# Kernel tuning notes

Hardware: AMD Instinct MI355X
Metric: run time of the kernel (lower is better)

Reference implementation:

```python
import jax, jax.numpy as jnp
from jax import lax
import numpy as np

PARAM_SPECS = [
    ("w1", (16, 15, 5, 5)), ("b1", (16,)),
    ("w2", (32, 16, 3, 3)), ("b2", (32,)),
    ("w3", (32, 32, 3, 3)), ("b3", (32,)),
    ("w4", (32, 32, 3, 3)), ("b4", (32,)),
    ("w5", (64, 32, 3, 3)), ("b5", (64,)),
    ("w6", (32, 96, 3, 3)), ("b6", (32,)),
    ("w7", (32, 64, 3, 3)), ("b7", (32,)),
    ("w8", (32, 64, 3, 3)), ("b8", (32,)),
    ("w9", (64, 48, 3, 3)), ("b9", (64,)),
    ("wi", (16, 15, 3, 3)), ("bi", (16,)),
    ("wo", (3, 16, 3, 3)), ("bo", (3,)),
]


def conv2d(x, w, b, pad):
    y = lax.conv_general_dilated(x, w, (1, 1), [(pad, pad), (pad, pad)],
                                 dimension_numbers=("NCHW", "OIHW", "NCHW"))
    return y + b[None, :, None, None]


def maxpool2(x):
    return lax.reduce_window(x, -jnp.inf, lax.max, (1, 1, 2, 2), (1, 1, 2, 2), "VALID")


def upsample(x, hw):
    # bilinear, half-pixel centers == torch align_corners=False
    B, C = x.shape[:2]
    return jax.image.resize(x, (B, C, hw[0], hw[1]), method="bilinear")


def dcnn(img, p):
    x1 = jax.nn.relu(conv2d(img, p["w1"], p["b1"], 2))
    x2 = jax.nn.relu(conv2d(maxpool2(x1), p["w2"], p["b2"], 1))
    x3 = jax.nn.relu(conv2d(maxpool2(x2), p["w3"], p["b3"], 1))
    x4 = jax.nn.relu(conv2d(maxpool2(x3), p["w4"], p["b4"], 1))
    x5 = jax.nn.relu(conv2d(maxpool2(x4), p["w5"], p["b5"], 1))
    x6 = jax.nn.relu(conv2d(jnp.concatenate([upsample(x5, x4.shape[-2:]), x4], 1), p["w6"], p["b6"], 1))
    x7 = jax.nn.relu(conv2d(jnp.concatenate([upsample(x6, x3.shape[-2:]), x3], 1), p["w7"], p["b7"], 1))
    x8 = jax.nn.relu(conv2d(jnp.concatenate([upsample(x7, x2.shape[-2:]), x2], 1), p["w8"], p["b8"], 1))
    x9 = conv2d(jnp.concatenate([upsample(x8, x1.shape[-2:]), x1], 1), p["w9"], p["b9"], 1)
    return x9


def lrnn_op(X, P, axis, flip):
    # h_k = (1-P_k)*X_k + P_k*h_{k-1}, scanned along `axis`.
    # For reverse directions the torch code stacks hidden states in scan
    # order (spatially flipped) -> flip inputs, scan forward, keep order.
    if flip:
        X = jnp.flip(X, axis)
        P = jnp.flip(P, axis)
    xs = jnp.moveaxis(X, axis, 0)  # [L, B, 16, n]
    ps = jnp.moveaxis(P, axis, 0)

    def step(h, xp):
        x, p = xp
        h = (1.0 - p) * x + p * h
        return h, h

    h0 = jnp.zeros_like(xs[0])
    _, ys = lax.scan(step, h0, (xs, ps))
    return jnp.moveaxis(ys, 0, axis)


def lrnn_layer(x_in, fm):
    dirs = [(0, 3, False), (0, 3, True), (16, 2, False), (16, 2, True),
            (32, 3, False), (32, 3, True), (48, 2, False), (48, 2, True)]
    outs = [lrnn_op(x_in, fm[:, c:c + 16], axis, flip) for (c, axis, flip) in dirs]
    return jnp.max(jnp.stack(outs, axis=1), axis=1)


def setup_inputs() -> dict:
    key = jax.random.key(0)
    ks = jax.random.split(key, len(PARAM_SPECS) + 1)
    inp = {"img": jax.random.normal(ks[0], (8, 15, 256, 256), jnp.float32)}
    for i, (name, shape) in enumerate(PARAM_SPECS):
        inp[name] = jax.random.normal(ks[i + 1], shape, jnp.float32) * 0.05
    return inp


def reference(img, w1, b1, w2, b2, w3, b3, w4, b4, w5, b5, w6, b6, w7, b7,
              w8, b8, w9, b9, wi, bi, wo, bo):
    p = dict(w1=w1, b1=b1, w2=w2, b2=b2, w3=w3, b3=b3, w4=w4, b4=b4, w5=w5,
             b5=b5, w6=w6, b6=b6, w7=w7, b7=b7, w8=w8, b8=b8, w9=w9, b9=b9)
    fm = jnp.tanh(dcnn(img, p))          # [B,64,H,W]
    x_in = conv2d(img, wi, bi, 1)         # [B,16,H,W]
    out = lrnn_layer(x_in, fm)            # [B,16,H,W]
    return jax.nn.sigmoid(conv2d(out, wo, bo, 1))  # [B,3,H,W]
```

## Files before the change

kernel.cpp:

```cpp
#include <hip/hip_runtime.h>
#include <math.h>

typedef __attribute__((ext_vector_type(8)))  short bf16x8;
typedef __attribute__((ext_vector_type(8)))  unsigned short u16x8;
typedef __attribute__((ext_vector_type(16))) float f32x16;

__device__ __forceinline__ unsigned short f2bf(float f) {
    unsigned u = __float_as_uint(f);
    unsigned r = (u + 0x7FFFu + ((u >> 16) & 1u)) >> 16;
    return (unsigned short)r;
}
__device__ __forceinline__ float bf2f(unsigned short h) {
    return __uint_as_float(((unsigned)h) << 16);
}
__device__ __forceinline__ unsigned pack2(unsigned short a, unsigned short b) {
    return (unsigned)a | ((unsigned)b << 16);
}
__device__ __forceinline__ float fast_tanh(float x) {
    float e = __expf(2.f * x);
    return 1.f - 2.f / (e + 1.f);
}

__device__ __forceinline__ void bilin_setup(int y, int x, int Hi, int Wi,
                                            int& i00, int& i01, int& i10, int& i11,
                                            float& wy, float& wx)
{
    float fy = 0.5f * y - 0.25f;
    float fx = 0.5f * x - 0.25f;
    float y0f = floorf(fy), x0f = floorf(fx);
    wy = fy - y0f; wx = fx - x0f;
    int yA = (int)y0f, xA = (int)x0f;
    int yB = yA + 1, xB = xA + 1;
    yA = yA < 0 ? 0 : (yA > Hi - 1 ? Hi - 1 : yA);
    yB = yB < 0 ? 0 : (yB > Hi - 1 ? Hi - 1 : yB);
    xA = xA < 0 ? 0 : (xA > Wi - 1 ? Wi - 1 : xA);
    xB = xB < 0 ? 0 : (xB > Wi - 1 ? Wi - 1 : xB);
    i00 = yA * Wi + xA; i01 = yA * Wi + xB;
    i10 = yB * Wi + xA; i11 = yB * Wi + xB;
}

__device__ __forceinline__ void up2_setup(int v, int Hi, int& i0, int& i1, float& w)
{
    int a = (v - 1) >> 1;
    i0 = a < 0 ? 0 : a;
    int b = a + 1;
    i1 = b > Hi - 1 ? Hi - 1 : b;
    w = (v & 1) ? 0.25f : 0.75f;
}

__device__ __forceinline__ u16x8 bilin8(const unsigned short* __restrict__ sb,
                                        int i00, int i01, int i10, int i11,
                                        float wy, float wx, int stride)
{
    u16x8 v00 = *(const u16x8*)(sb + (size_t)i00 * stride);
    u16x8 v01 = *(const u16x8*)(sb + (size_t)i01 * stride);
    u16x8 v10 = *(const u16x8*)(sb + (size_t)i10 * stride);
    u16x8 v11 = *(const u16x8*)(sb + (size_t)i11 * stride);
    float w00 = (1.f - wy) * (1.f - wx), w01 = (1.f - wy) * wx;
    float w10 = wy * (1.f - wx),         w11 = wy * wx;
    u16x8 r;
#pragma unroll
    for (int j = 0; j < 8; ++j)
        r[j] = f2bf(w00 * bf2f(v00[j]) + w01 * bf2f(v01[j]) +
                    w10 * bf2f(v10[j]) + w11 * bf2f(v11[j]));
    return r;
}

__global__ void imgT_bf16(const float* __restrict__ img, unsigned short* __restrict__ dst)
{
    int idx = blockIdx.x * 256 + threadIdx.x;
    if (idx >= 8 * 256 * 256) return;
    int x = idx & 255, y = (idx >> 8) & 255, b = idx >> 16;
    unsigned short v[16];
#pragma unroll
    for (int c = 0; c < 15; ++c)
        v[c] = f2bf(img[(size_t)(b * 15 + c) * 65536 + y * 256 + x]);
    v[15] = 0;
    uint4 lo = make_uint4(pack2(v[0], v[1]), pack2(v[2], v[3]), pack2(v[4], v[5]), pack2(v[6], v[7]));
    uint4 hi = make_uint4(pack2(v[8], v[9]), pack2(v[10], v[11]), pack2(v[12], v[13]), pack2(v[14], v[15]));
    *(uint4*)(dst + (size_t)idx * 16)     = lo;
    *(uint4*)(dst + (size_t)idx * 16 + 8) = hi;
}

__device__ __forceinline__ void pack33(const float* __restrict__ w,
                                       unsigned short* __restrict__ dst,
                                       int i, int Cin, int Cout)
{
    int KST = Cin >> 4, MT = Cout >> 5;
    int j = i & 7;
    int lane = (i >> 3) & 63;
    int t = i >> 9;
    int mt = t % MT; t /= MT;
    int kst = t % KST;
    int s = t / KST;
    int oc = mt * 32 + (lane & 31);
    int ci = kst * 16 + (lane >> 5) * 8 + j;
    dst[i] = f2bf(w[(oc * Cin + ci) * 9 + s]);
}

__global__ void wprep_mega(const float* __restrict__ w9, const float* __restrict__ w8,
                           const float* __restrict__ w1, const float* __restrict__ wi,
                           const float* __restrict__ wo, const float* __restrict__ w2,
                           const float* __restrict__ w3, const float* __restrict__ w4,
                           const float* __restrict__ w5, const float* __restrict__ w6,
                           const float* __restrict__ w7,
                           unsigned short* __restrict__ wpk9, unsigned short* __restrict__ wpk8,
                           unsigned short* __restrict__ wpk1, unsigned short* __restrict__ wpki,
                           unsigned short* __restrict__ wpko, unsigned short* __restrict__ wpk2,
                           unsigned short* __restrict__ wpk3, unsigned short* __restrict__ wpk4,
                           unsigned short* __restrict__ wpk5, unsigned short* __restrict__ wpk6,
                           unsigned short* __restrict__ wpk7)
{
    int idx = blockIdx.x * 256 + threadIdx.x;
    if (idx < 27648)       pack33(w9, wpk9, idx, 48, 64);
    else if (idx < 46080)  pack33(w8, wpk8, idx - 27648, 64, 32);
    else if (idx < 58880) {
        int i = idx - 46080;
        int j = i & 7;
        int lane = (i >> 3) & 63;
        int s = i >> 9;
        int oc = lane & 31;
        int ci = (lane >> 5) * 8 + j;
        float v = 0.f;
        if (oc < 16 && ci < 15) v = w1[((oc * 15 + ci) * 5 + s / 5) * 5 + s % 5];
        wpk1[i] = f2bf(v);
    } else if (idx < 63488) {
        int i = idx - 58880;
        int j = i & 7;
        int lane = (i >> 3) & 63;
        int s = i >> 9;
        int oc = lane & 31;
        int ci = (lane >> 5) * 8 + j;
        float v = 0.f;
        if (oc < 16 && ci < 15) v = wi[((oc * 15 + ci) * 3 + s / 3) * 3 + s % 3];
        wpki[i] = f2bf(v);
    } else if (idx < 68096) {
        int i = idx - 63488;
        int j = i & 7;
        int lane = (i >> 3) & 63;
        int s = i >> 9;
        int oc = lane & 31;
        int ci = (lane >> 5) * 8 + j;
        float v = 0.f;
        if (oc < 3) v = wo[((oc * 16 + ci) * 3 + s / 3) * 3 + s % 3];
        wpko[i] = f2bf(v);
    }
    else if (idx < 72704)  pack33(w2, wpk2, idx - 68096, 16, 32);
    else if (idx < 81920)  pack33(w3, wpk3, idx - 72704, 32, 32);
    else if (idx < 91136)  pack33(w4, wpk4, idx - 81920, 32, 32);
    else if (idx < 109568) pack33(w5, wpk5, idx - 91136, 32, 64);
    else if (idx < 137216) pack33(w6, wpk6, idx - 109568, 96, 32);
    else if (idx < 155648) pack33(w7, wpk7, idx - 137216, 64, 32);
}

template<int CIN, int COUT, int H, int W, int ROWS, int POOL>
__global__ __launch_bounds__(256)
void convN_mfma(const unsigned short* __restrict__ in,
                const unsigned short* __restrict__ wpk,
                const float* __restrict__ bias,
                unsigned short* __restrict__ out)
{
    constexpr int G = CIN / 8;
    constexpr int KST = CIN / 16;
    constexpr int MT = COUT / 32;
    constexpr int TR = ROWS + 2;
    constexpr int TWd = W + 2;
    constexpr int PS = TR * TWd * 8 + 8;
    __shared__ __align__(16) unsigned short smem[G * PS];

    const int tid  = threadIdx.x;
    const int lane = tid & 63;
    const int wv   = tid >> 6;
    const int q    = lane >> 5;
    const int y0   = blockIdx.x * ROWS;
    const int b    = blockIdx.y;

    for (int i = tid; i < G * TR * TWd; i += 256) {
        int g = i % G;
        int u = (i / G) % TWd;
        int t = i / (G * TWd);
        int yg = y0 + t - 1, xg = u - 1;
        u16x8 v = {0, 0, 0, 0, 0, 0, 0, 0};
        if (yg >= 0 && yg < H && xg >= 0 && xg < W) {
            if (POOL) {
                const unsigned short* q0 =
                    in + (((size_t)(b * 2 * H + 2 * yg) * 2 * W + 2 * xg) * CIN + g * 8);
                u16x8 a0 = *(const u16x8*)q0;
                u16x8 a1 = *(const u16x8*)(q0 + CIN);
                u16x8 a2 = *(const u16x8*)(q0 + (size_t)2 * W * CIN);
                u16x8 a3 = *(const u16x8*)(q0 + (size_t)2 * W * CIN + CIN);
#pragma unroll
                for (int j = 0; j < 8; ++j)
                    v[j] = f2bf(fmaxf(fmaxf(bf2f(a0[j]), bf2f(a1[j])),
                                      fmaxf(bf2f(a2[j]), bf2f(a3[j]))));
            } else {
                v = *(const u16x8*)(in + (((size_t)(b * H + yg) * W + xg) * CIN + g * 8));
            }
        }
        *(u16x8*)(&smem[g * PS + (t * TWd + u) * 8]) = v;
    }
    __syncthreads();

    const int p = wv * 32 + (lane & 31);
    const int r = p / W;
    const int x = p % W;

    f32x16 acc[MT];
#pragma unroll
    for (int mt = 0; mt < MT; ++mt)
#pragma unroll
        for (int i = 0; i < 16; ++i) acc[mt][i] = 0.f;

    const unsigned short* wbase = wpk + lane * 8;

#pragma unroll
    for (int s = 0; s < 9; ++s) {
        const int dy = s / 3, dx = s % 3;
#pragma unroll
        for (int kst = 0; kst < KST; ++kst) {
            const int g = kst * 2 + q;
            bf16x8 bfrag = *(const bf16x8*)(&smem[g * PS + ((r + dy) * TWd + (x + dx)) * 8]);
#pragma unroll
            for (int mt = 0; mt < MT; ++mt) {
                bf16x8 a = *(const bf16x8*)(wbase + ((s * KST + kst) * MT + mt) * 512);
                acc[mt] = __builtin_amdgcn_mfma_f32_32x32x16_bf16(a, bfrag, acc[mt], 0, 0, 0);
            }
        }
    }

    size_t base = ((size_t)(b * H + y0 + r) * W + x) * COUT;
#pragma unroll
    for (int mt = 0; mt < MT; ++mt)
#pragma unroll
        for (int rg = 0; rg < 4; ++rg) {
            int oc = mt * 32 + 8 * rg + 4 * q;
            unsigned short s0 = f2bf(fmaxf(acc[mt][rg * 4 + 0] + bias[oc + 0], 0.f));
            unsigned short s1 = f2bf(fmaxf(acc[mt][rg * 4 + 1] + bias[oc + 1], 0.f));
            unsigned short s2 = f2bf(fmaxf(acc[mt][rg * 4 + 2] + bias[oc + 2], 0.f));
            unsigned short s3 = f2bf(fmaxf(acc[mt][rg * 4 + 3] + bias[oc + 3], 0.f));
            *(uint2*)(out + base + oc) = make_uint2(pack2(s0, s1), pack2(s2, s3));
        }
}

template<int UPC, int CSKIP, int COUT, int H, int W, int ROWS>
__global__ __launch_bounds__(256)
void convU_mfma(const unsigned short* __restrict__ up,
                const unsigned short* __restrict__ skip,
                const unsigned short* __restrict__ wpk,
                const float* __restrict__ bias,
                unsigned short* __restrict__ out)
{
    constexpr int CIN = UPC + CSKIP;
    constexpr int G = CIN / 8;
    constexpr int GU = UPC / 8;
    constexpr int KST = CIN / 16;
    constexpr int MT = COUT / 32;
    constexpr int TR = ROWS + 2;
    constexpr int TWd = W + 2;
    constexpr int PS = TR * TWd * 8 + 8;
    __shared__ __align__(16) unsigned short smem[G * PS];

    const int tid  = threadIdx.x;
    const int lane = tid & 63;
    const int wv   = tid >> 6;
    const int q    = lane >> 5;
    const int y0   = blockIdx.x * ROWS;
    const int b    = blockIdx.y;

    for (int i = tid; i < G * TR * TWd; i += 256) {
        int g = i % G;
        int u = (i / G) % TWd;
        int t = i / (G * TWd);
        int yg = y0 + t - 1, xg = u - 1;
        u16x8 v = {0, 0, 0, 0, 0, 0, 0, 0};
        if (yg >= 0 && yg < H && xg >= 0 && xg < W) {
            if (g < GU) {
                int i00, i01, i10, i11; float wy, wx;
                bilin_setup(yg, xg, H / 2, W / 2, i00, i01, i10, i11, wy, wx);
                v = bilin8(up + (size_t)b * (H / 2) * (W / 2) * UPC + g * 8,
                           i00, i01, i10, i11, wy, wx, UPC);
            } else {
                v = *(const u16x8*)(skip + (((size_t)(b * H + yg) * W + xg) * CSKIP
                                            + (g - GU) * 8));
            }
        }
        *(u16x8*)(&smem[g * PS + (t * TWd + u) * 8]) = v;
    }
    __syncthreads();

    const int p = wv * 32 + (lane & 31);
    const int r = p / W;
    const int x = p % W;

    f32x16 acc[MT];
#pragma unroll
    for (int mt = 0; mt < MT; ++mt)
#pragma unroll
        for (int i = 0; i < 16; ++i) acc[mt][i] = 0.f;

    const unsigned short* wbase = wpk + lane * 8;

#pragma unroll
    for (int s = 0; s < 9; ++s) {
        const int dy = s / 3, dx = s % 3;
#pragma unroll
        for (int kst = 0; kst < KST; ++kst) {
            const int g = kst * 2 + q;
            bf16x8 bfrag = *(const bf16x8*)(&smem[g * PS + ((r + dy) * TWd + (x + dx)) * 8]);
#pragma unroll
            for (int mt = 0; mt < MT; ++mt) {
                bf16x8 a = *(const bf16x8*)(wbase + ((s * KST + kst) * MT + mt) * 512);
                acc[mt] = __builtin_amdgcn_mfma_f32_32x32x16_bf16(a, bfrag, acc[mt], 0, 0, 0);
            }
        }
    }

    size_t base = ((size_t)(b * H + y0 + r) * W + x) * COUT;
#pragma unroll
    for (int mt = 0; mt < MT; ++mt)
#pragma unroll
        for (int rg = 0; rg < 4; ++rg) {
            int oc = mt * 32 + 8 * rg + 4 * q;
            unsigned short s0 = f2bf(fmaxf(acc[mt][rg * 4 + 0] + bias[oc + 0], 0.f));
            unsigned short s1 = f2bf(fmaxf(acc[mt][rg * 4 + 1] + bias[oc + 1], 0.f));
            unsigned short s2 = f2bf(fmaxf(acc[mt][rg * 4 + 2] + bias[oc + 2], 0.f));
            unsigned short s3 = f2bf(fmaxf(acc[mt][rg * 4 + 3] + bias[oc + 3], 0.f));
            *(uint2*)(out + base + oc) = make_uint2(pack2(s0, s1), pack2(s2, s3));
        }
}

__global__ __launch_bounds__(256)
void conv1i_mfma(const unsigned short* __restrict__ imgT,
                 const unsigned short* __restrict__ wpk1,
                 const unsigned short* __restrict__ wpki,
                 const float* __restrict__ b1, const float* __restrict__ bi,
                 unsigned short* __restrict__ x1t, unsigned short* __restrict__ xin)
{
    __shared__ __align__(16) unsigned short smem[2 * 5 * 132 * 8];

    const int tid  = threadIdx.x;
    const int lane = tid & 63;
    const int wv   = tid >> 6;
    const int n    = lane & 31;
    const int q    = lane >> 5;
    const int y    = blockIdx.x >> 1;
    const int x0   = (blockIdx.x & 1) * 128;
    const int b    = blockIdx.y;

    for (int i = tid; i < 5 * 132 * 2; i += 256) {
        int r   = i / 264;
        int rem = i - r * 264;
        int xi  = rem >> 1;
        int g   = rem & 1;
        int yg = y + r - 2;
        int xg = x0 - 2 + xi;
        uint4 v = make_uint4(0, 0, 0, 0);
        if (yg >= 0 && yg < 256 && xg >= 0 && xg < 256)
            v = *(const uint4*)(imgT + (((size_t)(b * 256 + yg) * 256 + xg) * 16 + g * 8));
        *(uint4*)(&smem[((g * 5 + r) * 132 + xi) * 8]) = v;
    }
    __syncthreads();

    f32x16 acc1, acci;
#pragma unroll
    for (int i = 0; i < 16; ++i) { acc1[i] = 0.f; acci[i] = 0.f; }

    const int pxl = wv * 32 + n;
    const unsigned short* wb1 = wpk1 + lane * 8;
    const unsigned short* wbi = wpki + lane * 8;

#pragma unroll
    for (int s = 0; s < 25; ++s) {
        const int dy = s / 5, dx = s % 5;
        bf16x8 bfrag = *(const bf16x8*)(&smem[((q * 5 + dy) * 132 + pxl + dx) * 8]);
        bf16x8 a = *(const bf16x8*)(wb1 + s * 512);
        acc1 = __builtin_amdgcn_mfma_f32_32x32x16_bf16(a, bfrag, acc1, 0, 0, 0);
    }
#pragma unroll
    for (int s = 0; s < 9; ++s) {
        const int dy = s / 3, dx = s % 3;
        bf16x8 bfrag = *(const bf16x8*)(&smem[((q * 5 + dy + 1) * 132 + pxl + dx + 1) * 8]);
        bf16x8 a = *(const bf16x8*)(wbi + s * 512);
        acci = __builtin_amdgcn_mfma_f32_32x32x16_bf16(a, bfrag, acci, 0, 0, 0);
    }

    const int px = x0 + pxl;
    size_t base1 = ((size_t)(b * 256 + y) * 256 + px) * 16;
#pragma unroll
    for (int rg = 0; rg < 2; ++rg) {
        int oc = 8 * rg + 4 * q;
        unsigned short s0 = f2bf(fmaxf(acc1[rg * 4 + 0] + b1[oc + 0], 0.f));
        unsigned short s1 = f2bf(fmaxf(acc1[rg * 4 + 1] + b1[oc + 1], 0.f));
        unsigned short s2 = f2bf(fmaxf(acc1[rg * 4 + 2] + b1[oc + 2], 0.f));
        unsigned short s3 = f2bf(fmaxf(acc1[rg * 4 + 3] + b1[oc + 3], 0.f));
        *(uint2*)(x1t + base1 + oc) = make_uint2(pack2(s0, s1), pack2(s2, s3));
    }
#pragma unroll
    for (int reg = 0; reg < 8; ++reg) {
        int row = (reg & 3) + 8 * (reg >> 2) + 4 * q;
        xin[((size_t)(b * 16 + row) * 256 + y) * 256 + px] = f2bf(acci[reg] + bi[row]);
    }
}

__global__ __launch_bounds__(256)
void conv8_mfma(const unsigned short* __restrict__ x7t,
                const unsigned short* __restrict__ x2t,
                const unsigned short* __restrict__ wpk8,
                const float* __restrict__ bias,
                unsigned short* __restrict__ x8t)
{
    constexpr int PS8 = 4 * 66 * 8 + 8;
    __shared__ __align__(16) unsigned short smem[8 * PS8];

    const int tid  = threadIdx.x;
    const int lane = tid & 63;
    const int wv   = tid >> 6;
    const int n    = lane & 31;
    const int q    = lane >> 5;
    const int x0   = (blockIdx.x & 1) * 64;
    const int yp   = blockIdx.x >> 1;
    const int b    = blockIdx.y;

    for (int i = tid; i < 8 * 4 * 66; i += 256) {
        int t   = i / 528;
        int rem = i - t * 528;
        int xi  = rem >> 3;
        int g   = rem & 7;
        int yg = 2 * yp + t - 1;
        int xg = x0 - 1 + xi;
        u16x8 v = {0, 0, 0, 0, 0, 0, 0, 0};
        if (yg >= 0 && yg < 128 && xg >= 0 && xg < 128) {
            if (g < 4) {
                int iy0, iy1, ix0, ix1; float wy, wx;
                up2_setup(yg, 64, iy0, iy1, wy);
                up2_setup(xg, 64, ix0, ix1, wx);
                v = bilin8(x7t + (size_t)b * 64 * 64 * 32 + g * 8,
                           iy0 * 64 + ix0, iy0 * 64 + ix1,
                           iy1 * 64 + ix0, iy1 * 64 + ix1, wy, wx, 32);
            } else {
                v = *(const u16x8*)(x2t + (((size_t)(b * 128 + yg) * 128 + xg) * 32
                                           + (g - 4) * 8));
            }
        }
        *(u16x8*)(&smem[g * PS8 + (t * 66 + xi) * 8]) = v;
    }
    __syncthreads();

    const int rr  = wv >> 1;
    const int pxl = (wv & 1) * 32 + n;

    f32x16 acc;
#pragma unroll
    for (int i = 0; i < 16; ++i) acc[i] = 0.f;

    const unsigned short* wbase = wpk8 + lane * 8;

#pragma unroll
    for (int s = 0; s < 9; ++s) {
        const int dy = s / 3, dx = s % 3;
#pragma unroll
        for (int kst = 0; kst < 4; ++kst) {
            const int g = kst * 2 + q;
            bf16x8 bfrag = *(const bf16x8*)(&smem[g * PS8 + ((rr + dy) * 66 + pxl + dx) * 8]);
            bf16x8 a = *(const bf16x8*)(wbase + (s * 4 + kst) * 512);
            acc = __builtin_amdgcn_mfma_f32_32x32x16_bf16(a, bfrag, acc, 0, 0, 0);
        }
    }

    size_t base = ((size_t)(b * 128 + 2 * yp + rr) * 128 + x0 + pxl) * 32;
#pragma unroll
    for (int rg = 0; rg < 4; ++rg) {
        int oc0 = 8 * rg + 4 * q;
        unsigned short s0 = f2bf(fmaxf(acc[rg * 4 + 0] + bias[oc0 + 0], 0.f));
        unsigned short s1 = f2bf(fmaxf(acc[rg * 4 + 1] + bias[oc0 + 1], 0.f));
        unsigned short s2 = f2bf(fmaxf(acc[rg * 4 + 2] + bias[oc0 + 2], 0.f));
        unsigned short s3 = f2bf(fmaxf(acc[rg * 4 + 3] + bias[oc0 + 3], 0.f));
        *(uint2*)(x8t + base + oc0) = make_uint2(pack2(s0, s1), pack2(s2, s3));
    }
}

__global__ __launch_bounds__(256)
void conv9f_mfma(const unsigned short* __restrict__ x8t,
                 const unsigned short* __restrict__ x1t,
                 const unsigned short* __restrict__ wpk,
                 const float* __restrict__ bias,
                 unsigned short* __restrict__ fm)
{
    constexpr int PS9 = 4 * 66 * 8 + 8;
    __shared__ __align__(16) unsigned short smem[6 * PS9];

    const int tid  = threadIdx.x;
    const int lane = tid & 63;
    const int wv   = tid >> 6;
    const int n    = lane & 31;
    const int q    = lane >> 5;
    const int x0   = (blockIdx.x & 3) * 64;
    const int yp   = blockIdx.x >> 2;
    const int b    = blockIdx.y;

    for (int i = tid; i < 6 * 4 * 66; i += 256) {
        int t   = i / 396;
        int rem = i - t * 396;
        int xi  = rem / 6;
        int g   = rem - xi * 6;
        int yg = 2 * yp + t - 1;
        int xg = x0 - 1 + xi;
        u16x8 v = {0, 0, 0, 0, 0, 0, 0, 0};
        if (yg >= 0 && yg < 256 && xg >= 0 && xg < 256) {
            if (g < 4) {
                int iy0, iy1, ix0, ix1; float wy, wx;
                up2_setup(yg, 128, iy0, iy1, wy);
                up2_setup(xg, 128, ix0, ix1, wx);
                v = bilin8(x8t + (size_t)b * 128 * 128 * 32 + g * 8,
                           iy0 * 128 + ix0, iy0 * 128 + ix1,
                           iy1 * 128 + ix0, iy1 * 128 + ix1, wy, wx, 32);
            } else {
                v = *(const u16x8*)(x1t + (((size_t)(b * 256 + yg) * 256 + xg) * 16 + (g - 4) * 8));
            }
        }
        *(u16x8*)(&smem[g * PS9 + (t * 66 + xi) * 8]) = v;
    }
    __syncthreads();

    const int rr  = wv >> 1;
    const int pxl = (wv & 1) * 32 + n;

    f32x16 acc0, acc1;
#pragma unroll
    for (int i = 0; i < 16; ++i) { acc0[i] = 0.f; acc1[i] = 0.f; }

    const unsigned short* wbase = wpk + lane * 8;

#pragma unroll
    for (int s = 0; s < 9; ++s) {
        const int dy = s / 3, dx = s % 3;
#pragma unroll
        for (int kst = 0; kst < 3; ++kst) {
            const int g = kst * 2 + q;
            bf16x8 bfrag = *(const bf16x8*)(&smem[g * PS9 + ((rr + dy) * 66 + pxl + dx) * 8]);
            bf16x8 a0 = *(const bf16x8*)(wbase + ((s * 3 + kst) * 2 + 0) * 512);
            bf16x8 a1 = *(const bf16x8*)(wbase + ((s * 3 + kst) * 2 + 1) * 512);
            acc0 = __builtin_amdgcn_mfma_f32_32x32x16_bf16(a0, bfrag, acc0, 0, 0, 0);
            acc1 = __builtin_amdgcn_mfma_f32_32x32x16_bf16(a1, bfrag, acc1, 0, 0, 0);
        }
    }

    __syncthreads();
    unsigned short* lout = smem;
    const int pb = rr * 64 + pxl + q * 512;
#pragma unroll
    for (int reg = 0; reg < 16; ++reg) {
        const int rbase = (reg & 3) + 8 * (reg >> 2);
        lout[rbase * 128 + pb]        = f2bf(fast_tanh(acc0[reg] + bias[rbase + 4 * q]));
        lout[(rbase + 32) * 128 + pb] = f2bf(fast_tanh(acc1[reg] + bias[rbase + 4 * q + 32]));
    }
    __syncthreads();

    const size_t fmb = (size_t)b * 64 * 65536 + (size_t)(2 * yp) * 256 + x0;
    for (int i = tid; i < 1024; i += 256) {
        int oc  = i >> 4;
        int p0  = (i & 15) * 8;
        int rr2 = p0 >> 6;
        int pl  = p0 & 63;
        uint4 v = *(const uint4*)(lout + oc * 128 + p0);
        *(uint4*)(fm + fmb + (size_t)oc * 65536 + rr2 * 256 + pl) = v;
    }
}

__device__ __forceinline__ int X2C(int x) { return x + (x >> 5); }

__global__ __launch_bounds__(256)
void lrnn_w_seg(const unsigned short* __restrict__ X, const unsigned short* __restrict__ FM,
                unsigned short* __restrict__ rnnW)
{
    __shared__ float tx[3][16][264];
    __shared__ unsigned short outm[2][16][256];
    __shared__ float segres[2][16][8][4];
    __shared__ float hin[2][16][8][2];

    const int tid = threadIdx.x;
    const int bid = blockIdx.x;
    const int yt = bid & 15;
    const int c  = (bid >> 4) & 15;
    const int b  = bid >> 8;
    const int y0 = yt * 16;

    const size_t xb  = ((size_t)(b * 16 + c) * 256 + y0) * 256;
    const size_t p1b = ((size_t)(b * 64 + c) * 256 + y0) * 256;
    const size_t p2b = ((size_t)(b * 64 + 32 + c) * 256 + y0) * 256;

    for (int i = tid; i < 1536; i += 256) {
        int s = i >> 9;
        int r = i & 511;
        int y = r >> 5;
        int g = r & 31;
        const unsigned short* sp = (s == 0) ? (X + xb) : (s == 1 ? FM + p1b : FM + p2b);
        u16x8 v = *(const u16x8*)(sp + (size_t)y * 256 + g * 8);
        int c0 = X2C(g * 8);
#pragma unroll
        for (int j = 0; j < 8; ++j) tx[s][y][c0 + j] = bf2f(v[j]);
    }
    __syncthreads();

    const int y  = tid & 15;
    const int sg = (tid >> 4) & 7;
    const int d  = tid >> 7;

    {
        float h1 = 0.f, h2 = 0.f, A1 = 1.f, A2 = 1.f;
        if (d == 0) {
            int cs = X2C(sg * 32);
#pragma unroll
            for (int i = 0; i < 32; ++i) {
                float xv = tx[0][y][cs + i], p1 = tx[1][y][cs + i], p2 = tx[2][y][cs + i];
                h1 = fmaf(p1, h1 - xv, xv); A1 *= p1;
                h2 = fmaf(p2, h2 - xv, xv); A2 *= p2;
            }
        } else {
            int cs = X2C(255 - sg * 32);
#pragma unroll
            for (int i = 0; i < 32; ++i) {
                float xv = tx[0][y][cs - i], p1 = tx[1][y][cs - i], p2 = tx[2][y][cs - i];
                h1 = fmaf(p1, h1 - xv, xv); A1 *= p1;
                h2 = fmaf(p2, h2 - xv, xv); A2 *= p2;
            }
        }
        segres[d][y][sg][0] = h1; segres[d][y][sg][1] = A1;
        segres[d][y][sg][2] = h2; segres[d][y][sg][3] = A2;
    }
    __syncthreads();

    if (tid < 32) {
        int yy = tid & 15, dd = tid >> 4;
        float c1 = 0.f, c2 = 0.f;
        for (int s = 0; s < 8; ++s) {
            hin[dd][yy][s][0] = c1;
            hin[dd][yy][s][1] = c2;
            c1 = segres[dd][yy][s][0] + segres[dd][yy][s][1] * c1;
            c2 = segres[dd][yy][s][2] + segres[dd][yy][s][3] * c2;
        }
    }
    __syncthreads();

    {
        float h1 = hin[d][y][sg][0], h2 = hin[d][y][sg][1];
        if (d == 0) {
            int cs = X2C(sg * 32);
            int xs = sg * 32;
#pragma unroll
            for (int i = 0; i < 32; ++i) {
                float xv = tx[0][y][cs + i], p1 = tx[1][y][cs + i], p2 = tx[2][y][cs + i];
                h1 = fmaf(p1, h1 - xv, xv);
                h2 = fmaf(p2, h2 - xv, xv);
                outm[0][y][xs + i] = f2bf(fmaxf(h1, h2));
            }
        } else {
            int cs = X2C(255 - sg * 32);
#pragma unroll
            for (int i = 0; i < 32; ++i) {
                int t = sg * 32 + i;
                float xv = tx[0][y][cs - i], p1 = tx[1][y][cs - i], p2 = tx[2][y][cs - i];
                h1 = fmaf(p1, h1 - xv, xv);
                h2 = fmaf(p2, h2 - xv, xv);
                outm[1][y][t] = f2bf(fmaxf(h1, h2));
            }
        }
    }
    __syncthreads();

    for (int i = tid; i < 4096; i += 256) {
        int x = i & 255, yy = i >> 8;
        float m = fmaxf(bf2f(outm[0][yy][x]), bf2f(outm[1][yy][x]));
        rnnW[xb + (size_t)yy * 256 + x] = f2bf(m);
    }
}

__global__ __launch_bounds__(256)
void lrnn_h_seg(const unsigned short* __restrict__ X, const unsigned short* __restrict__ FM,
                unsigned short* __restrict__ rnnH)
{
    __shared__ float tx[3][264][17];
    __shared__ unsigned short outm[2][256][16];
    __shared__ float segres[2][16][8][4];
    __shared__ float hin[2][16][8][2];

    const int tid = threadIdx.x;
    const int bid = blockIdx.x;
    const int xt = bid & 15;
    const int c  = (bid >> 4) & 15;
    const int b  = bid >> 8;
    const int x0 = xt * 16;

    const size_t xb  = (size_t)(b * 16 + c) * 65536 + x0;
    const size_t p1b = (size_t)(b * 64 + 16 + c) * 65536 + x0;
    const size_t p2b = (size_t)(b * 64 + 48 + c) * 65536 + x0;

    for (int i = tid; i < 1536; i += 256) {
        int s = i >> 9;
        int r = i & 511;
        int y = r >> 1;
        int g = r & 1;
        const unsigned short* sp = (s == 0) ? (X + xb) : (s == 1 ? FM + p1b : FM + p2b);
        u16x8 v = *(const u16x8*)(sp + (size_t)y * 256 + g * 8);
        int pr = y + (y >> 5);
#pragma unroll
        for (int j = 0; j < 8; ++j) tx[s][pr][g * 8 + j] = bf2f(v[j]);
    }
    __syncthreads();

    const int x  = tid & 15;
    const int sg = (tid >> 4) & 7;
    const int d  = tid >> 7;

    {
        float h1 = 0.f, h2 = 0.f, A1 = 1.f, A2 = 1.f;
        if (d == 0) {
            int rs = X2C(sg * 32);
#pragma unroll
            for (int i = 0; i < 32; ++i) {
                float xv = tx[0][rs + i][x], p1 = tx[1][rs + i][x], p2 = tx[2][rs + i][x];
                h1 = fmaf(p1, h1 - xv, xv); A1 *= p1;
                h2 = fmaf(p2, h2 - xv, xv); A2 *= p2;
            }
        } else {
            int rs = X2C(255 - sg * 32);
#pragma unroll
            for (int i = 0; i < 32; ++i) {
                float xv = tx[0][rs - i][x], p1 = tx[1][rs - i][x], p2 = tx[2][rs - i][x];
                h1 = fmaf(p1, h1 - xv, xv); A1 *= p1;
                h2 = fmaf(p2, h2 - xv, xv); A2 *= p2;
            }
        }
        segres[d][x][sg][0] = h1; segres[d][x][sg][1] = A1;
        segres[d][x][sg][2] = h2; segres[d][x][sg][3] = A2;
    }
    __syncthreads();

    if (tid < 32) {
        int xx = tid & 15, dd = tid >> 4;
        float c1 = 0.f, c2 = 0.f;
        for (int s = 0; s < 8; ++s) {
            hin[dd][xx][s][0] = c1;
            hin[dd][xx][s][1] = c2;
            c1 = segres[dd][xx][s][0] + segres[dd][xx][s][1] * c1;
            c2 = segres[dd][xx][s][2] + segres[dd][xx][s][3] * c2;
        }
    }
    __syncthreads();

    {
        float h1 = hin[d][x][sg][0], h2 = hin[d][x][sg][1];
        if (d == 0) {
            int rs = X2C(sg * 32);
            int ys = sg * 32;
#pragma unroll
            for (int i = 0; i < 32; ++i) {
                float xv = tx[0][rs + i][x], p1 = tx[1][rs + i][x], p2 = tx[2][rs + i][x];
                h1 = fmaf(p1, h1 - xv, xv);
                h2 = fmaf(p2, h2 - xv, xv);
                outm[0][ys + i][x] = f2bf(fmaxf(h1, h2));
            }
        } else {
            int rs = X2C(255 - sg * 32);
#pragma unroll
            for (int i = 0; i < 32; ++i) {
                int t = sg * 32 + i;
                float xv = tx[0][rs - i][x], p1 = tx[1][rs - i][x], p2 = tx[2][rs - i][x];
                h1 = fmaf(p1, h1 - xv, xv);
                h2 = fmaf(p2, h2 - xv, xv);
                outm[1][t][x] = f2bf(fmaxf(h1, h2));
            }
        }
    }
    __syncthreads();

    for (int i = tid; i < 4096; i += 256) {
        int xx = i & 15, yy = i >> 4;
        float m = fmaxf(bf2f(outm[0][yy][xx]), bf2f(outm[1][yy][xx]));
        rnnH[xb + (size_t)yy * 256 + xx] = f2bf(m);
    }
}

__global__ __launch_bounds__(256)
void convo_mfma(const unsigned short* __restrict__ rnnW,
                const unsigned short* __restrict__ rnnH,
                const unsigned short* __restrict__ wpko,
                const float* __restrict__ bo,
                float* __restrict__ outp)
{
    __shared__ __align__(16) unsigned short smem[2 * 3 * 130 * 8];

    const int tid  = threadIdx.x;
    const int lane = tid & 63;
    const int wv   = tid >> 6;
    const int n    = lane & 31;
    const int q    = lane >> 5;
    const int y    = blockIdx.x >> 1;
    const int x0   = (blockIdx.x & 1) * 128;
    const int b    = blockIdx.y;

    for (int i = tid; i < 3 * 16 * 130; i += 256) {
        int xi = i % 130;
        int t  = i / 130;
        int ch = t & 15;
        int r  = t >> 4;
        int yg = y + r - 1;
        int xg = x0 - 1 + xi;
        unsigned short m = 0;
        if (yg >= 0 && yg < 256 && xg >= 0 && xg < 256) {
            size_t off = (size_t)(b * 16 + ch) * 65536 + yg * 256 + xg;
            m = f2bf(fmaxf(bf2f(rnnW[off]), bf2f(rnnH[off])));
        }
        int g = ch >> 3, j = ch & 7;
        smem[((g * 3 + r) * 130 + xi) * 8 + j] = m;
    }
    __syncthreads();

    f32x16 acc;
#pragma unroll
    for (int i = 0; i < 16; ++i) acc[i] = 0.f;

    const int pxl = wv * 32 + n;
    const unsigned short* wbase = wpko + lane * 8;

#pragma unroll
    for (int s = 0; s < 9; ++s) {
        const int dy = s / 3, dx = s % 3;
        bf16x8 bfrag = *(const bf16x8*)(&smem[((q * 3 + dy) * 130 + pxl + dx) * 8]);
        bf16x8 a = *(const bf16x8*)(wbase + s * 512);
        acc = __builtin_amdgcn_mfma_f32_32x32x16_bf16(a, bfrag, acc, 0, 0, 0);
    }

    const int px = x0 + pxl;
    if (q == 0) {
#pragma unroll
        for (int oc = 0; oc < 3; ++oc) {
            float r = acc[oc] + bo[oc];
            outp[((size_t)(b * 3 + oc) * 256 + y) * 256 + px] = 1.f / (1.f + __expf(-r));
        }
    }
}

extern "C" void kernel_launch(void* const* d_in, const int* in_sizes, int n_in,
                              void* d_out, int out_size, void* d_ws, size_t ws_size,
                              hipStream_t stream)
{
    const float* img = (const float*)d_in[0];
    const float* w1 = (const float*)d_in[1];  const float* b1 = (const float*)d_in[2];
    const float* w2 = (const float*)d_in[3];  const float* b2 = (const float*)d_in[4];
    const float* w3 = (const float*)d_in[5];  const float* b3 = (const float*)d_in[6];
    const float* w4 = (const float*)d_in[7];  const float* b4 = (const float*)d_in[8];
    const float* w5 = (const float*)d_in[9];  const float* b5 = (const float*)d_in[10];
    const float* w6 = (const float*)d_in[11]; const float* b6 = (const float*)d_in[12];
    const float* w7 = (const float*)d_in[13]; const float* b7 = (const float*)d_in[14];
    const float* w8 = (const float*)d_in[15]; const float* b8 = (const float*)d_in[16];
    const float* w9 = (const float*)d_in[17]; const float* b9 = (const float*)d_in[18];
    const float* wi = (const float*)d_in[19]; const float* bi = (const float*)d_in[20];
    const float* wo = (const float*)d_in[21]; const float* bo = (const float*)d_in[22];

    char* wsb = (char*)d_ws;
    const size_t MB = (size_t)(1u << 20);
    unsigned short* imgT  = (unsigned short*)(wsb);
    unsigned short* x1t   = (unsigned short*)(wsb + 16 * MB);
    unsigned short* x2t   = (unsigned short*)(wsb + 32 * MB);
    unsigned short* x3t   = (unsigned short*)(wsb + 40 * MB);
    unsigned short* x4t   = (unsigned short*)(wsb + 42 * MB);
    unsigned short* x5t   = (unsigned short*)(wsb + 43 * MB);
    unsigned short* x6t   = (unsigned short*)(wsb + 46 * MB);
    unsigned short* x7t   = (unsigned short*)(wsb + 51 * MB);
    unsigned short* x8t   = (unsigned short*)(wsb + 70 * MB);
    unsigned short* fm16  = (unsigned short*)(wsb + 112 * MB);
    unsigned short* xin16 = (unsigned short*)(wsb + 176 * MB);
    unsigned short* rnnW  = (unsigned short*)(wsb);
    unsigned short* rnnH  = (unsigned short*)(wsb + 16 * MB);
    unsigned short* wpk9 = (unsigned short*)(wsb + 192 * MB);
    unsigned short* wpk8 = wpk9 + 27648;
    unsigned short* wpk1 = wpk8 + 18432;
    unsigned short* wpki = wpk1 + 12800;
    unsigned short* wpko = wpki + 4608;
    unsigned short* wpk2 = wpko + 4608;
    unsigned short* wpk3 = wpk2 + 4608;
    unsigned short* wpk4 = wpk3 + 9216;
    unsigned short* wpk5 = wpk4 + 9216;
    unsigned short* wpk6 = wpk5 + 18432;
    unsigned short* wpk7 = wpk6 + 27648;
    float* outp = (float*)d_out;

    wprep_mega<<<608, 256, 0, stream>>>(w9, w8, w1, wi, wo, w2, w3, w4, w5, w6, w7,
                                        wpk9, wpk8, wpk1, wpki, wpko,
                                        wpk2, wpk3, wpk4, wpk5, wpk6, wpk7);
    imgT_bf16<<<2048, 256, 0, stream>>>(img, imgT);

    { dim3 grd(512, 8);
      conv1i_mfma<<<grd, 256, 0, stream>>>(imgT, wpk1, wpki, b1, bi, x1t, xin16); }

    convN_mfma<16, 32, 128, 128, 1, 1><<<dim3(128, 8), 256, 0, stream>>>(x1t, wpk2, b2, x2t);
    convN_mfma<32, 32, 64, 64, 2, 1><<<dim3(32, 8), 256, 0, stream>>>(x2t, wpk3, b3, x3t);
    convN_mfma<32, 32, 32, 32, 4, 1><<<dim3(8, 8), 256, 0, stream>>>(x3t, wpk4, b4, x4t);
    convN_mfma<32, 64, 16, 16, 8, 1><<<dim3(2, 8), 256, 0, stream>>>(x4t, wpk5, b5, x5t);

    convU_mfma<64, 32, 32, 32, 32, 4><<<dim3(8, 8), 256, 0, stream>>>(x5t, x4t, wpk6, b6, x6t);
    convU_mfma<32, 32, 32, 64, 64, 2><<<dim3(32, 8), 256, 0, stream>>>(x6t, x3t, wpk7, b7, x7t);
    { dim3 grd(128, 8);
      conv8_mfma<<<grd, 256, 0, stream>>>(x7t, x2t, wpk8, b8, x8t); }

    { dim3 grd(512, 8);
      conv9f_mfma<<<grd, 256, 0, stream>>>(x8t, x1t, wpk9, b9, fm16); }

    lrnn_w_seg<<<2048, 256, 0, stream>>>(xin16, fm16, rnnW);
    lrnn_h_seg<<<2048, 256, 0, stream>>>(xin16, fm16, rnnH);

    { dim3 grd(512, 8);
      convo_mfma<<<grd, 256, 0, stream>>>(rnnW, rnnH, wpko, bo, outp); }
}
```

Before: 400.7 us.

## Fold vertical bilinear upsample into conv9 weights for x8 channels

Instead of bilinearly upsampling x8 in both directions before conv9, the vertical interpolation is folded into per-row-parity and per-boundary-class effective weights, precomputed in the weight prep kernel. The conv9 tile now stages only horizontally interpolated low-resolution x8 rows (3 rows instead of 4 upsampled ones), which cuts global gathers and interpolation math in the staging loop. It adds six weight variant sets (more weight memory and L2 traffic) and a larger prep launch, and it changes bf16 rounding points slightly.

```diff
diff --git a/kernel.cpp b/kernel.cpp
--- a/kernel.cpp
+++ b/kernel.cpp
@@ -66,6 +66,15 @@
     return r;
 }
 
+__device__ const float ALPH[3][2][3][3] = {
+    { { {0.f,0.f,0.f},      {0.f,1.f,0.f},       {0.f,0.75f,0.25f} },
+      { {0.f,1.f,0.f},      {0.f,0.75f,0.25f},   {0.f,0.25f,0.75f} } },
+    { { {0.75f,0.25f,0.f},  {0.25f,0.75f,0.f},   {0.f,0.75f,0.25f} },
+      { {0.25f,0.75f,0.f},  {0.f,0.75f,0.25f},   {0.f,0.25f,0.75f} } },
+    { { {0.75f,0.25f,0.f},  {0.25f,0.75f,0.f},   {0.f,1.f,0.f} },
+      { {0.25f,0.75f,0.f},  {0.f,1.f,0.f},       {0.f,0.f,0.f} } }
+};
+
 __global__ void imgT_bf16(const float* __restrict__ img, unsigned short* __restrict__ dst)
 {
     int idx = blockIdx.x * 256 + threadIdx.x;
@@ -109,7 +118,7 @@
                            unsigned short* __restrict__ wpko, unsigned short* __restrict__ wpk2,
                            unsigned short* __restrict__ wpk3, unsigned short* __restrict__ wpk4,
                            unsigned short* __restrict__ wpk5, unsigned short* __restrict__ wpk6,
-                           unsigned short* __restrict__ wpk7)
+                           unsigned short* __restrict__ wpk7, unsigned short* __restrict__ wpk9e)
 {
     int idx = blockIdx.x * 256 + threadIdx.x;
     if (idx < 27648)       pack33(w9, wpk9, idx, 48, 64);
@@ -151,6 +160,25 @@
     else if (idx < 109568) pack33(w5, wpk5, idx - 91136, 32, 64);
     else if (idx < 137216) pack33(w6, wpk6, idx - 109568, 96, 32);
     else if (idx < 155648) pack33(w7, wpk7, idx - 137216, 64, 32);
+    else if (idx < 266240) {
+        int i = idx - 155648;
+        int j = i & 7;
+        int lane = (i >> 3) & 63;
+        int t = i >> 9;
+        int half = t & 1; t >>= 1;
+        int kst  = t & 1; t >>= 1;
+        int s    = t % 9; t /= 9;
+        int py   = t & 1;
+        int cls  = t >> 1;
+        int dr = s / 3, dx = s % 3;
+        int oc = half * 32 + (lane & 31);
+        int ci = kst * 16 + (lane >> 5) * 8 + j;
+        float v = 0.f;
+#pragma unroll
+        for (int dy = 0; dy < 3; ++dy)
+            v += ALPH[cls][py][dy][dr] * w9[((oc * 48 + ci) * 3 + dy) * 3 + dx];
+        wpk9e[i] = f2bf(v);
+    }
 }
 
 template<int CIN, int COUT, int H, int W, int ROWS, int POOL>
@@ -483,11 +511,14 @@
 void conv9f_mfma(const unsigned short* __restrict__ x8t,
                  const unsigned short* __restrict__ x1t,
                  const unsigned short* __restrict__ wpk,
+                 const unsigned short* __restrict__ wpk9e,
                  const float* __restrict__ bias,
                  unsigned short* __restrict__ fm)
 {
-    constexpr int PS9 = 4 * 66 * 8 + 8;
-    __shared__ __align__(16) unsigned short smem[6 * PS9];
+    constexpr int PS8X = 3 * 66 * 8 + 8;
+    constexpr int PS1  = 4 * 66 * 8 + 8;
+    constexpr int X1OFF = 4 * PS8X;
+    __shared__ __align__(16) unsigned short smem[4 * PS8X + 2 * PS1];
 
     const int tid  = threadIdx.x;
     const int lane = tid & 63;
@@ -498,27 +529,40 @@
     const int yp   = blockIdx.x >> 2;
     const int b    = blockIdx.y;
 
-    for (int i = tid; i < 6 * 4 * 66; i += 256) {
-        int t   = i / 396;
-        int rem = i - t * 396;
-        int xi  = rem / 6;
-        int g   = rem - xi * 6;
-        int yg = 2 * yp + t - 1;
-        int xg = x0 - 1 + xi;
-        u16x8 v = {0, 0, 0, 0, 0, 0, 0, 0};
-        if (yg >= 0 && yg < 256 && xg >= 0 && xg < 256) {
-            if (g < 4) {
-                int iy0, iy1, ix0, ix1; float wy, wx;
-                up2_setup(yg, 128, iy0, iy1, wy);
+    for (int i = tid; i < 792 + 528; i += 256) {
+        if (i < 792) {
+            int g   = i & 3;
+            int rem = i >> 2;
+            int xi  = rem % 66;
+            int t8  = rem / 66;
+            int r   = yp - 1 + t8;
+            int xg  = x0 - 1 + xi;
+            u16x8 v = {0, 0, 0, 0, 0, 0, 0, 0};
+            if (r >= 0 && r < 128 && xg >= 0 && xg < 256) {
+                int ix0, ix1; float wx;
                 up2_setup(xg, 128, ix0, ix1, wx);
-                v = bilin8(x8t + (size_t)b * 128 * 128 * 32 + g * 8,
-                           iy0 * 128 + ix0, iy0 * 128 + ix1,
-                           iy1 * 128 + ix0, iy1 * 128 + ix1, wy, wx, 32);
-            } else {
-                v = *(const u16x8*)(x1t + (((size_t)(b * 256 + yg) * 256 + xg) * 16 + (g - 4) * 8));
-            }
-        }
-        *(u16x8*)(&smem[g * PS9 + (t * 66 + xi) * 8]) = v;
+                const unsigned short* S = x8t + ((size_t)(b * 128 + r) * 128) * 32 + g * 8;
+                u16x8 a0 = *(const u16x8*)(S + ix0 * 32);
+                u16x8 a1 = *(const u16x8*)(S + ix1 * 32);
+                float w1x = 1.f - wx;
+#pragma unroll
+                for (int j = 0; j < 8; ++j)
+                    v[j] = f2bf(w1x * bf2f(a0[j]) + wx * bf2f(a1[j]));
+            }
+            *(u16x8*)(&smem[g * PS8X + (t8 * 66 + xi) * 8]) = v;
+        } else {
+            int jI  = i - 792;
+            int g   = jI & 1;
+            int rem = jI >> 1;
+            int xi  = rem % 66;
+            int t   = rem / 66;
+            int yg  = 2 * yp + t - 1;
+            int xg  = x0 - 1 + xi;
+            uint4 v = make_uint4(0, 0, 0, 0);
+            if (yg >= 0 && yg < 256 && xg >= 0 && xg < 256)
+                v = *(const uint4*)(x1t + (((size_t)(b * 256 + yg) * 256 + xg) * 16 + g * 8));
+            *(uint4*)(&smem[X1OFF + g * PS1 + (t * 66 + xi) * 8]) = v;
+        }
     }
     __syncthreads();
 
@@ -529,17 +573,26 @@
 #pragma unroll
     for (int i = 0; i < 16; ++i) { acc0[i] = 0.f; acc1[i] = 0.f; }
 
-    const unsigned short* wbase = wpk + lane * 8;
+    const int cls = (yp == 0) ? 0 : ((yp == 127) ? 2 : 1);
+    const unsigned short* wE  = wpk9e + (size_t)(cls * 2 + rr) * 18432 + lane * 8;
+    const unsigned short* w2b = wpk + lane * 8;
 
 #pragma unroll
     for (int s = 0; s < 9; ++s) {
-        const int dy = s / 3, dx = s % 3;
-#pragma unroll
-        for (int kst = 0; kst < 3; ++kst) {
+        const int dr = s / 3, dxx = s % 3;
+#pragma unroll
+        for (int kst = 0; kst < 2; ++kst) {
             const int g = kst * 2 + q;
-            bf16x8 bfrag = *(const bf16x8*)(&smem[g * PS9 + ((rr + dy) * 66 + pxl + dx) * 8]);
-            bf16x8 a0 = *(const bf16x8*)(wbase + ((s * 3 + kst) * 2 + 0) * 512);
-            bf16x8 a1 = *(const bf16x8*)(wbase + ((s * 3 + kst) * 2 + 1) * 512);
+            bf16x8 bfrag = *(const bf16x8*)(&smem[g * PS8X + (dr * 66 + pxl + dxx) * 8]);
+            bf16x8 a0 = *(const bf16x8*)(wE + ((s * 2 + kst) * 2 + 0) * 512);
+            bf16x8 a1 = *(const bf16x8*)(wE + ((s * 2 + kst) * 2 + 1) * 512);
+            acc0 = __builtin_amdgcn_mfma_f32_32x32x16_bf16(a0, bfrag, acc0, 0, 0, 0);
+            acc1 = __builtin_amdgcn_mfma_f32_32x32x16_bf16(a1, bfrag, acc1, 0, 0, 0);
+        }
+        {
+            bf16x8 bfrag = *(const bf16x8*)(&smem[X1OFF + q * PS1 + ((rr + dr) * 66 + pxl + dxx) * 8]);
+            bf16x8 a0 = *(const bf16x8*)(w2b + ((s * 3 + 2) * 2 + 0) * 512);
+            bf16x8 a1 = *(const bf16x8*)(w2b + ((s * 3 + 2) * 2 + 1) * 512);
             acc0 = __builtin_amdgcn_mfma_f32_32x32x16_bf16(a0, bfrag, acc0, 0, 0, 0);
             acc1 = __builtin_amdgcn_mfma_f32_32x32x16_bf16(a1, bfrag, acc1, 0, 0, 0);
         }
@@ -884,11 +937,12 @@
     unsigned short* wpk5 = wpk4 + 9216;
     unsigned short* wpk6 = wpk5 + 18432;
     unsigned short* wpk7 = wpk6 + 27648;
+    unsigned short* wpk9e = wpk7 + 18432;
     float* outp = (float*)d_out;
 
-    wprep_mega<<<608, 256, 0, stream>>>(w9, w8, w1, wi, wo, w2, w3, w4, w5, w6, w7,
-                                        wpk9, wpk8, wpk1, wpki, wpko,
-                                        wpk2, wpk3, wpk4, wpk5, wpk6, wpk7);
+    wprep_mega<<<1040, 256, 0, stream>>>(w9, w8, w1, wi, wo, w2, w3, w4, w5, w6, w7,
+                                         wpk9, wpk8, wpk1, wpki, wpko,
+                                         wpk2, wpk3, wpk4, wpk5, wpk6, wpk7, wpk9e);
     imgT_bf16<<<2048, 256, 0, stream>>>(img, imgT);
 
     { dim3 grd(512, 8);
@@ -905,7 +959,7 @@
       conv8_mfma<<<grd, 256, 0, stream>>>(x7t, x2t, wpk8, b8, x8t); }
 
     { dim3 grd(512, 8);
-      conv9f_mfma<<<grd, 256, 0, stream>>>(x8t, x1t, wpk9, b9, fm16); }
+      conv9f_mfma<<<grd, 256, 0, stream>>>(x8t, x1t, wpk9, wpk9e, b9, fm16); }
 
     lrnn_w_seg<<<2048, 256, 0, stream>>>(xin16, fm16, rnnW);
     lrnn_h_seg<<<2048, 256, 0, stream>>>(xin16, fm16, rnnH);
```

New measurement: 387.0 us. 3.4% less time.
